# Optimization experiments

Measured on AMD Instinct MI355X. Metric: run time of the kernel, lower is better.

Reference implementation:

```python
import jax, jax.numpy as jnp
import numpy as np

# CTBG circuit dims: units=[512,512,512], action_sz=6
UNIT1, UNIT2, UNIT3, ACTION = 512, 512, 512, 6
D_GPE_IN = UNIT1 * 3          # 1536  (striatum D1/D2/D3 blocks)
D_GPE_OUT = UNIT2 * 3         # 1536
D_GPI_IN = (UNIT1 + UNIT2) * 3  # 3072 (striatum + GPe/STN blocks)
D_GPI_OUT = UNIT2 * 3         # 1536
B = 16384


def setup_inputs() -> dict:
    key = jax.random.key(0)
    ks = jax.random.split(key, 12)
    x = jax.random.normal(ks[0], (B, D_GPE_IN), jnp.float32)
    # per-unit diagonal connectivity masks (unit_diags): [units, input_dim]
    gpe_mask = jax.random.bernoulli(ks[1], 0.5, (D_GPE_OUT, D_GPE_IN)).astype(jnp.float32)
    gpi_mask = jax.random.bernoulli(ks[2], 0.5, (D_GPI_OUT, D_GPI_IN)).astype(jnp.float32)
    # non-negative weights, uniform [0, 0.01) as in the TF initializer
    gpe_w = jax.random.uniform(ks[3], (D_GPE_IN, D_GPE_OUT), jnp.float32, 0.0, 0.01)
    gpe_b = jnp.zeros((D_GPE_OUT,), jnp.float32)
    gpi_w = jax.random.uniform(ks[4], (D_GPI_IN, D_GPI_OUT), jnp.float32, 0.0, 0.01)
    gpi_b = jnp.zeros((D_GPI_OUT,), jnp.float32)
    # Motor_cortex dense stack
    w1 = jax.random.normal(ks[5], (D_GPI_OUT, UNIT3), jnp.float32) / np.sqrt(D_GPI_OUT)
    b1 = jnp.zeros((UNIT3,), jnp.float32)
    w2 = jax.random.normal(ks[6], (UNIT3, UNIT3), jnp.float32) / np.sqrt(UNIT3)
    b2 = jnp.zeros((UNIT3,), jnp.float32)
    w3 = jax.random.normal(ks[7], (UNIT3, ACTION), jnp.float32) / np.sqrt(UNIT3)
    b3 = jnp.zeros((ACTION,), jnp.float32)
    return {"x": x, "gpe_mask": gpe_mask, "gpe_w": gpe_w, "gpe_b": gpe_b,
            "gpi_mask": gpi_mask, "gpi_w": gpi_w, "gpi_b": gpi_b,
            "w1": w1, "b1": b1, "w2": w2, "b2": b2, "w3": w3, "b3": b3}


def _masked_layer(x, mask, w, b):
    # TF original: p = transpose(matmul(diag(mask_u), x^T)) -> [B,U,I];
    #              f = diag_part(matmul(p, w)) + b
    # algebraically: f[b,u] = sum_i mask[u,i] * x[b,i] * w[i,u] + b[u]
    # which is a plain matmul against the element-wise masked weight.
    return x @ (w * mask.T) + b


def reference(x, gpe_mask, gpe_w, gpe_b, gpi_mask, gpi_w, gpi_b,
              w1, b1, w2, b2, w3, b3):
    gpe_out = _masked_layer(x, gpe_mask, gpe_w, gpe_b)          # [B, 1536]
    gpi_in = jnp.concatenate([x, gpe_out], axis=-1)              # [B, 3072]
    gpi_out = _masked_layer(gpi_in, gpi_mask, gpi_w, gpi_b)      # [B, 1536]
    h = jax.nn.relu(gpi_out @ w1 + b1)
    h = jax.nn.relu(h @ w2 + b2)
    return jax.nn.relu(h @ w3 + b3)                              # [B, 6]
```

## Files before the change

### kernel.cpp

```cpp
#include <hip/hip_runtime.h>
#include <stdint.h>


typedef __attribute__((ext_vector_type(8))) short short8;
typedef __attribute__((ext_vector_type(4))) float floatx4;

typedef const __attribute__((address_space(1))) void* gas1_cvp;
typedef __attribute__((address_space(3))) void* gas3_vp;

__device__ __forceinline__ void load_lds16(const void* g, void* s) {
    __builtin_amdgcn_global_load_lds((gas1_cvp)g, (gas3_vp)s, 16, 0, 0);
}

__device__ __forceinline__ unsigned short f2bf(float f) {
    unsigned int u = __float_as_uint(f);
    u = u + 0x7fffu + ((u >> 16) & 1u);
    return (unsigned short)(u >> 16);
}
__device__ __forceinline__ float bf2f(unsigned short h) {
    return __uint_as_float(((unsigned int)h) << 16);
}
__device__ __forceinline__ short8 cvt8(float4 a, float4 b) {
    short8 r;
    r[0] = (short)f2bf(a.x); r[1] = (short)f2bf(a.y);
    r[2] = (short)f2bf(a.z); r[3] = (short)f2bf(a.w);
    r[4] = (short)f2bf(b.x); r[5] = (short)f2bf(b.y);
    r[6] = (short)f2bf(b.z); r[7] = (short)f2bf(b.w);
    return r;
}

__device__ __forceinline__ void dev_prep_t(
        float (*tile)[65],
        const float* __restrict__ w, const float* __restrict__ mask,
        unsigned short* __restrict__ out,
        int ldw, int ldm, int ldo, int bx, int by) {
    int n0 = bx * 64;
    int k0 = by * 64;
    int t = threadIdx.x;
    int c4 = (t & 15) * 4;
    int r  = t >> 4;

    #pragma unroll
    for (int p = 0; p < 4; ++p) {
        int kk = r + p * 16;
        float4 v = *(const float4*)(w + (size_t)(k0 + kk) * ldw + n0 + c4);
        tile[c4 + 0][kk] = v.x;
        tile[c4 + 1][kk] = v.y;
        tile[c4 + 2][kk] = v.z;
        tile[c4 + 3][kk] = v.w;
    }
    __syncthreads();
    #pragma unroll
    for (int p = 0; p < 4; ++p) {
        int nn = r + p * 16;
        float mx = 1.f, my = 1.f, mz = 1.f, mw = 1.f;
        if (mask) {
            float4 m = *(const float4*)(mask + (size_t)(n0 + nn) * ldm + k0 + c4);
            mx = m.x; my = m.y; mz = m.z; mw = m.w;
        }
        ushort4 o;
        o.x = f2bf(tile[nn][c4 + 0] * mx);
        o.y = f2bf(tile[nn][c4 + 1] * my);
        o.z = f2bf(tile[nn][c4 + 2] * mz);
        o.w = f2bf(tile[nn][c4 + 3] * mw);
        *(ushort4*)(out + (size_t)(n0 + nn) * ldo + k0 + c4) = o;
    }
}

__device__ __forceinline__ void dev_prep_nt(
        float (*tile)[65],
        const float* __restrict__ w, const float* __restrict__ mask,
        unsigned short* __restrict__ out,
        int ldw, int ldm, int ldo, int bx, int by) {
    int j0 = bx * 64;
    int i0 = by * 64;
    int t = threadIdx.x;
    int c4 = (t & 15) * 4;
    int r  = t >> 4;

    #pragma unroll
    for (int p = 0; p < 4; ++p) {
        int jj = r + p * 16;
        float4 m = *(const float4*)(mask + (size_t)(j0 + jj) * ldm + i0 + c4);
        tile[c4 + 0][jj] = m.x;
        tile[c4 + 1][jj] = m.y;
        tile[c4 + 2][jj] = m.z;
        tile[c4 + 3][jj] = m.w;
    }
    __syncthreads();
    #pragma unroll
    for (int p = 0; p < 4; ++p) {
        int ii = r + p * 16;
        float4 v = *(const float4*)(w + (size_t)(i0 + ii) * ldw + j0 + c4);
        ushort4 o;
        o.x = f2bf(v.x * tile[ii][c4 + 0]);
        o.y = f2bf(v.y * tile[ii][c4 + 1]);
        o.z = f2bf(v.z * tile[ii][c4 + 2]);
        o.w = f2bf(v.w * tile[ii][c4 + 3]);
        *(ushort4*)(out + (size_t)(i0 + ii) * ldo + j0 + c4) = o;
    }
}

__global__ __launch_bounds__(256) void prep_all_kernel(
        const float* __restrict__ gpe_w, const float* __restrict__ gpe_mask,
        const float* __restrict__ gpi_w, const float* __restrict__ gpi_mask,
        const float* __restrict__ w1, const float* __restrict__ w2,
        unsigned short* __restrict__ wi_topnt, unsigned short* __restrict__ wi_bot,
        unsigned short* __restrict__ we_nt, unsigned short* __restrict__ w1t,
        unsigned short* __restrict__ w2t) {
    __shared__ float tile[64][65];
    int b = blockIdx.x;
    if (b < 576) {
        dev_prep_nt(tile, gpi_w, gpi_mask, wi_topnt, 1536, 3072, 1536,
                    b % 24, b / 24);
    } else if (b < 1152) {
        int lb = b - 576;
        dev_prep_t(tile, gpi_w + (size_t)1536 * 1536, gpi_mask + 1536, wi_bot,
                   1536, 3072, 1536, lb % 24, lb / 24);
    } else if (b < 1728) {
        int lb = b - 1152;
        dev_prep_nt(tile, gpe_w, gpe_mask, we_nt, 1536, 1536, 1536,
                    lb % 24, lb / 24);
    } else if (b < 1920) {
        int lb = b - 1728;
        dev_prep_t(tile, w1, nullptr, w1t, 512, 0, 1536, lb % 8, lb / 8);
    } else {
        int lb = b - 1920;
        dev_prep_t(tile, w2, nullptr, w2t, 512, 0, 512, lb % 8, lb / 8);
    }
}

__device__ __forceinline__ void dev_bvec(
        const float* __restrict__ avec, const float* __restrict__ base,
        const unsigned short* __restrict__ wbt, float* __restrict__ outv,
        int K, int ld, int blk) {
    int u = blk * 4 + (threadIdx.x >> 6);
    int lane = threadIdx.x & 63;
    const unsigned short* rowp = wbt + (size_t)u * ld;
    float s = 0.f;
    for (int j = lane; j < K; j += 64) s += avec[j] * bf2f(rowp[j]);
    #pragma unroll
    for (int off = 32; off; off >>= 1) s += __shfl_down(s, off, 64);
    if (lane == 0) outv[u] = base[u] + s;
}

template <int BMODE>
__device__ __forceinline__ void dev_gemm64(
        unsigned short* As, unsigned short* Bs,
        const unsigned short* __restrict__ A,
        const unsigned short* __restrict__ Bt,
        const unsigned short* __restrict__ Add,
        unsigned short* __restrict__ C,
        int K, int lda, int ldc, int bx, int by) {
    const int m0 = by * 64;
    const int n0 = bx * 64;
    const int t    = threadIdx.x;
    const int lane = t & 63;
    const int w    = t >> 6;
    const int wm   = w >> 1;
    const int wn   = w & 1;
    const int lm   = lane & 15;
    const int lq   = lane >> 4;

    const int srow = lane >> 2;
    const int scol = (lane & 3) * 8;
    const unsigned short* ag = A  + (size_t)(m0 + w * 16 + srow) * lda + scol;
    const unsigned short* bg = Bt + (size_t)(n0 + w * 16 + srow) * K + scol;
    unsigned short* sA = As + w * 512;
    unsigned short* sB = Bs + w * 512;

    const unsigned short* arp[2];
    const unsigned short* brp[2];
    #pragma unroll
    for (int i = 0; i < 2; ++i) {
        arp[i] = As + (wm * 32 + i * 16 + lm) * 32 + lq * 8;
        brp[i] = Bs + (wn * 32 + i * 16 + lm) * 32 + lq * 8;
    }

    floatx4 acc[2][2] = {};

    for (int k0 = 0; k0 < K; k0 += 32) {
        __syncthreads();
        load_lds16(ag + k0, sA);
        load_lds16(bg + k0, sB);
        __syncthreads();

        short8 af[2], bf8[2];
        #pragma unroll
        for (int i = 0; i < 2; ++i) {
            af[i]  = *(const short8*)arp[i];
            bf8[i] = *(const short8*)brp[i];
        }
        #pragma unroll
        for (int mi = 0; mi < 2; ++mi)
            #pragma unroll
            for (int ni = 0; ni < 2; ++ni)
                acc[mi][ni] = __builtin_amdgcn_mfma_f32_16x16x32_bf16(
                    af[mi], bf8[ni], acc[mi][ni], 0, 0, 0);
    }

    #pragma unroll
    for (int mi = 0; mi < 2; ++mi) {
        int rbase = m0 + wm * 32 + mi * 16 + lq * 4;
        #pragma unroll
        for (int ni = 0; ni < 2; ++ni) {
            int cc = n0 + wn * 32 + ni * 16 + lm;
            #pragma unroll
            for (int r = 0; r < 4; ++r) {
                float v = acc[mi][ni][r];
                if (BMODE == 1) v += bf2f(Add[(size_t)(rbase + r) * ldc + cc]);
                C[(size_t)(rbase + r) * ldc + cc] = f2bf(v);
            }
        }
    }
}

__global__ __launch_bounds__(256) void combo1_kernel(
        const unsigned short* __restrict__ we_nt,
        const unsigned short* __restrict__ wi_bot,
        const unsigned short* __restrict__ wi_topnt,
        unsigned short* __restrict__ wc_nt,
        const float* __restrict__ gpe_b, const float* __restrict__ gpi_b,
        float* __restrict__ bc) {
    __shared__ unsigned short As[64 * 32];
    __shared__ unsigned short Bs[64 * 32];
    int b = blockIdx.x;
    if (b < 576) {
        dev_gemm64<1>(As, Bs, we_nt, wi_bot, wi_topnt, wc_nt,
                      1536, 1536, 1536, b % 24, b / 24);
    } else {
        dev_bvec(gpe_b, gpi_b, wi_bot, bc, 1536, 1536, b - 576);
    }
}

__global__ __launch_bounds__(256) void combo2_kernel(
        const unsigned short* __restrict__ w1t,
        const unsigned short* __restrict__ wc_nt,
        unsigned short* __restrict__ w1ct,
        const float* __restrict__ bc, const float* __restrict__ b1,
        float* __restrict__ b1c) {
    __shared__ unsigned short As[64 * 32];
    __shared__ unsigned short Bs[64 * 32];
    int b = blockIdx.x;
    if (b < 192) {
        dev_gemm64<2>(As, Bs, w1t, wc_nt, nullptr, w1ct,
                      1536, 1536, 1536, b % 24, b / 24);
    } else {
        dev_bvec(bc, b1, w1t, b1c, 1536, 1536, b - 192);
    }
}

__global__ __launch_bounds__(256) void gemm_a32_kernel(
        const float* __restrict__ A,
        const unsigned short* __restrict__ Bt,
        const float* __restrict__ bias,
        unsigned short* __restrict__ C,
        int K, int lda, int ldc) {
    __shared__ unsigned short As[128 * 32];
    __shared__ unsigned short Bs[128 * 32];

    const int m0 = blockIdx.y * 128;
    const int n0 = blockIdx.x * 128;
    const int t    = threadIdx.x;
    const int lane = t & 63;
    const int w    = t >> 6;
    const int wm   = w >> 1;
    const int wn   = w & 1;
    const int lm   = lane & 15;
    const int lq   = lane >> 4;

    const int srow = lane >> 2;
    const int scol = (lane & 3) * 8;
    const float* axg0 = A + (size_t)(m0 + w * 16 + srow) * lda + scol;
    const float* axg1 = A + (size_t)(m0 + (4 + w) * 16 + srow) * lda + scol;
    const unsigned short* bg0 = Bt + (size_t)(n0 + w * 16 + srow) * K + scol;
    const unsigned short* bg1 = Bt + (size_t)(n0 + (4 + w) * 16 + srow) * K + scol;
    unsigned short* sA0w = As + (w * 16 + srow) * 32 + scol;
    unsigned short* sA1w = As + ((4 + w) * 16 + srow) * 32 + scol;
    unsigned short* sB0 = Bs + w * 512;
    unsigned short* sB1 = Bs + (4 + w) * 512;

    const unsigned short* arp[4];
    const unsigned short* brp[4];
    #pragma unroll
    for (int i = 0; i < 4; ++i) {
        arp[i] = As + (wm * 64 + i * 16 + lm) * 32 + lq * 8;
        brp[i] = Bs + (wn * 64 + i * 16 + lm) * 32 + lq * 8;
    }

    floatx4 acc[4][4] = {};

    for (int k0 = 0; k0 < K; k0 += 32) {
        float4 a00 = *(const float4*)(axg0 + k0);
        float4 a01 = *(const float4*)(axg0 + k0 + 4);
        float4 a10 = *(const float4*)(axg1 + k0);
        float4 a11 = *(const float4*)(axg1 + k0 + 4);
        __syncthreads();
        load_lds16(bg0 + k0, sB0);
        load_lds16(bg1 + k0, sB1);
        *(short8*)sA0w = cvt8(a00, a01);
        *(short8*)sA1w = cvt8(a10, a11);
        __syncthreads();

        short8 af[4], bf8[4];
        #pragma unroll
        for (int i = 0; i < 4; ++i) {
            af[i]  = *(const short8*)arp[i];
            bf8[i] = *(const short8*)brp[i];
        }
        #pragma unroll
        for (int mi = 0; mi < 4; ++mi)
            #pragma unroll
            for (int ni = 0; ni < 4; ++ni)
                acc[mi][ni] = __builtin_amdgcn_mfma_f32_16x16x32_bf16(
                    af[mi], bf8[ni], acc[mi][ni], 0, 0, 0);
    }

    float bv[4];
    #pragma unroll
    for (int ni = 0; ni < 4; ++ni) bv[ni] = bias[n0 + wn * 64 + ni * 16 + lm];

    #pragma unroll
    for (int mi = 0; mi < 4; ++mi) {
        int rbase = m0 + wm * 64 + mi * 16 + lq * 4;
        #pragma unroll
        for (int ni = 0; ni < 4; ++ni) {
            int cc = n0 + wn * 64 + ni * 16 + lm;
            #pragma unroll
            for (int r = 0; r < 4; ++r) {
                float v = fmaxf(acc[mi][ni][r] + bv[ni], 0.f);
                C[(size_t)(rbase + r) * ldc + cc] = f2bf(v);
            }
        }
    }
}

__global__ __launch_bounds__(256) void gemm_bt_kernel(
        const unsigned short* __restrict__ A,
        const unsigned short* __restrict__ Bt,
        const float* __restrict__ bias,
        unsigned short* __restrict__ C,
        int K, int lda, int ldc) {
    __shared__ unsigned short As[128 * 32];
    __shared__ unsigned short Bs[128 * 32];

    const int m0 = blockIdx.y * 128;
    const int n0 = blockIdx.x * 128;
    const int t    = threadIdx.x;
    const int lane = t & 63;
    const int w    = t >> 6;
    const int wm   = w >> 1;
    const int wn   = w & 1;
    const int lm   = lane & 15;
    const int lq   = lane >> 4;

    const int srow = lane >> 2;
    const int scol = (lane & 3) * 8;
    const unsigned short* ag0 = A  + (size_t)(m0 + w * 16 + srow) * lda + scol;
    const unsigned short* ag1 = A  + (size_t)(m0 + (4 + w) * 16 + srow) * lda + scol;
    const unsigned short* bg0 = Bt + (size_t)(n0 + w * 16 + srow) * K + scol;
    const unsigned short* bg1 = Bt + (size_t)(n0 + (4 + w) * 16 + srow) * K + scol;
    unsigned short* sA0 = As + w * 512;
    unsigned short* sA1 = As + (4 + w) * 512;
    unsigned short* sB0 = Bs + w * 512;
    unsigned short* sB1 = Bs + (4 + w) * 512;

    const unsigned short* arp[4];
    const unsigned short* brp[4];
    #pragma unroll
    for (int i = 0; i < 4; ++i) {
        arp[i] = As + (wm * 64 + i * 16 + lm) * 32 + lq * 8;
        brp[i] = Bs + (wn * 64 + i * 16 + lm) * 32 + lq * 8;
    }

    floatx4 acc[4][4] = {};

    for (int k0 = 0; k0 < K; k0 += 32) {
        __syncthreads();
        load_lds16(ag0 + k0, sA0);
        load_lds16(ag1 + k0, sA1);
        load_lds16(bg0 + k0, sB0);
        load_lds16(bg1 + k0, sB1);
        __syncthreads();

        short8 af[4], bf8[4];
        #pragma unroll
        for (int i = 0; i < 4; ++i) {
            af[i]  = *(const short8*)arp[i];
            bf8[i] = *(const short8*)brp[i];
        }
        #pragma unroll
        for (int mi = 0; mi < 4; ++mi)
            #pragma unroll
            for (int ni = 0; ni < 4; ++ni)
                acc[mi][ni] = __builtin_amdgcn_mfma_f32_16x16x32_bf16(
                    af[mi], bf8[ni], acc[mi][ni], 0, 0, 0);
    }

    float bv[4];
    #pragma unroll
    for (int ni = 0; ni < 4; ++ni) bv[ni] = bias[n0 + wn * 64 + ni * 16 + lm];

    #pragma unroll
    for (int mi = 0; mi < 4; ++mi) {
        int rbase = m0 + wm * 64 + mi * 16 + lq * 4;
        #pragma unroll
        for (int ni = 0; ni < 4; ++ni) {
            int cc = n0 + wn * 64 + ni * 16 + lm;
            #pragma unroll
            for (int r = 0; r < 4; ++r) {
                float v = fmaxf(acc[mi][ni][r] + bv[ni], 0.f);
                C[(size_t)(rbase + r) * ldc + cc] = f2bf(v);
            }
        }
    }
}

__global__ void head_kernel(const unsigned short* __restrict__ h,
                            const float* __restrict__ w3,
                            const float* __restrict__ b3,
                            float* __restrict__ out) {
    int row = blockIdx.x * 4 + (threadIdx.x >> 6);
    int lane = threadIdx.x & 63;
    const unsigned short* hp = h + (size_t)row * 512 + lane * 8;
    ushort4 ha = *(const ushort4*)(hp);
    ushort4 hb = *(const ushort4*)(hp + 4);
    float hv[8] = {bf2f(ha.x), bf2f(ha.y), bf2f(ha.z), bf2f(ha.w),
                   bf2f(hb.x), bf2f(hb.y), bf2f(hb.z), bf2f(hb.w)};
    const float* wp = w3 + lane * 48;
    float s[6] = {0.f, 0.f, 0.f, 0.f, 0.f, 0.f};
    #pragma unroll
    for (int j = 0; j < 8; ++j)
        #pragma unroll
        for (int a = 0; a < 6; ++a)
            s[a] += hv[j] * wp[j * 6 + a];
    #pragma unroll
    for (int a = 0; a < 6; ++a)
        #pragma unroll
        for (int off = 32; off; off >>= 1)
            s[a] += __shfl_down(s[a], off, 64);
    if (lane == 0) {
        #pragma unroll
        for (int a = 0; a < 6; ++a)
            out[(size_t)row * 6 + a] = fmaxf(s[a] + b3[a], 0.f);
    }
}

extern "C" void kernel_launch(void* const* d_in, const int* in_sizes, int n_in,
                              void* d_out, int out_size, void* d_ws, size_t ws_size,
                              hipStream_t stream) {
    const float* x        = (const float*)d_in[0];
    const float* gpe_mask = (const float*)d_in[1];
    const float* gpe_w    = (const float*)d_in[2];
    const float* gpe_b    = (const float*)d_in[3];
    const float* gpi_mask = (const float*)d_in[4];
    const float* gpi_w    = (const float*)d_in[5];
    const float* gpi_b    = (const float*)d_in[6];
    const float* w1       = (const float*)d_in[7];
    const float* b1       = (const float*)d_in[8];
    const float* w2       = (const float*)d_in[9];
    const float* b2       = (const float*)d_in[10];
    const float* w3       = (const float*)d_in[11];
    const float* b3       = (const float*)d_in[12];
    float* out = (float*)d_out;

    char* ws = (char*)d_ws;
    unsigned short* h1        = (unsigned short*)(ws);
    unsigned short* h2        = (unsigned short*)(ws + 16777216);
    unsigned short* wi_topnt  = (unsigned short*)(ws + 33554432);
    unsigned short* wi_bot    = (unsigned short*)(ws + 38273024);
    unsigned short* we_nt     = (unsigned short*)(ws + 42991616);
    unsigned short* wc_nt     = (unsigned short*)(ws + 47710208);
    unsigned short* w1t       = (unsigned short*)(ws + 52428800);
    unsigned short* w2t       = (unsigned short*)(ws + 54001664);
    unsigned short* w1ct      = (unsigned short*)(ws + 54525952);
    float*          bc        = (float*)(ws + 56098816);
    float*          b1c       = (float*)(ws + 56104960);

    prep_all_kernel<<<dim3(1984), dim3(256), 0, stream>>>(
        gpe_w, gpe_mask, gpi_w, gpi_mask, w1, w2,
        wi_topnt, wi_bot, we_nt, w1t, w2t);

    combo1_kernel<<<dim3(960), dim3(256), 0, stream>>>(
        we_nt, wi_bot, wi_topnt, wc_nt, gpe_b, gpi_b, bc);

    combo2_kernel<<<dim3(320), dim3(256), 0, stream>>>(
        w1t, wc_nt, w1ct, bc, b1, b1c);

    gemm_a32_kernel<<<dim3(4, 128), dim3(256), 0, stream>>>(
        x, w1ct, b1c, h1, 1536, 1536, 512);
    gemm_bt_kernel<<<dim3(4, 128), dim3(256), 0, stream>>>(
        h1, w2t, b2, h2, 512, 512, 512);
    head_kernel<<<dim3(16384 / 4), dim3(256), 0, stream>>>(h2, w3, b3, out);
}
```

Before: 334.4 us.

## Retile fp32-input GEMM to full-width 32-row blocks so x is read once

Replaces the 128x128-tiled first GEMM, which read and converted each x row four times (once per N tile), with blocks covering 32 rows and all 512 output columns. Each x element is now read from fp32 global memory and converted to bf16 only once, and the next A chunk is prefetched into registers while the current one is processed. The trade-off is that every block streams the full 512x1536 weight matrix through LDS (32 KB of B per k-step), so weight traffic per row rises and only 512 blocks are launched, which lowers parallelism.

```diff
diff --git a/kernel.cpp b/kernel.cpp
--- a/kernel.cpp
+++ b/kernel.cpp
@@ -19,14 +19,6 @@
 }
 __device__ __forceinline__ float bf2f(unsigned short h) {
     return __uint_as_float(((unsigned int)h) << 16);
-}
-__device__ __forceinline__ short8 cvt8(float4 a, float4 b) {
-    short8 r;
-    r[0] = (short)f2bf(a.x); r[1] = (short)f2bf(a.y);
-    r[2] = (short)f2bf(a.z); r[3] = (short)f2bf(a.w);
-    r[4] = (short)f2bf(b.x); r[5] = (short)f2bf(b.y);
-    r[6] = (short)f2bf(b.z); r[7] = (short)f2bf(b.w);
-    return r;
 }
 
 __device__ __forceinline__ void dev_prep_t(
@@ -250,86 +242,79 @@
     }
 }
 
-__global__ __launch_bounds__(256) void gemm_a32_kernel(
+__global__ __launch_bounds__(256) void gemm_x32_kernel(
         const float* __restrict__ A,
         const unsigned short* __restrict__ Bt,
         const float* __restrict__ bias,
-        unsigned short* __restrict__ C,
-        int K, int lda, int ldc) {
-    __shared__ unsigned short As[128 * 32];
-    __shared__ unsigned short Bs[128 * 32];
-
-    const int m0 = blockIdx.y * 128;
-    const int n0 = blockIdx.x * 128;
+        unsigned short* __restrict__ C) {
+    __shared__ unsigned short As[32 * 32];
+    __shared__ unsigned short Bs[512 * 32];
+
+    const int m0   = blockIdx.x * 32;
     const int t    = threadIdx.x;
     const int lane = t & 63;
     const int w    = t >> 6;
-    const int wm   = w >> 1;
-    const int wn   = w & 1;
     const int lm   = lane & 15;
     const int lq   = lane >> 4;
 
+    const int arow = t >> 3;
+    const int acol = (t & 7) * 4;
+    const float* ag = A + (size_t)(m0 + arow) * 1536 + acol;
+    unsigned short* sAw = As + arow * 32 + acol;
+
     const int srow = lane >> 2;
     const int scol = (lane & 3) * 8;
-    const float* axg0 = A + (size_t)(m0 + w * 16 + srow) * lda + scol;
-    const float* axg1 = A + (size_t)(m0 + (4 + w) * 16 + srow) * lda + scol;
-    const unsigned short* bg0 = Bt + (size_t)(n0 + w * 16 + srow) * K + scol;
-    const unsigned short* bg1 = Bt + (size_t)(n0 + (4 + w) * 16 + srow) * K + scol;
-    unsigned short* sA0w = As + (w * 16 + srow) * 32 + scol;
-    unsigned short* sA1w = As + ((4 + w) * 16 + srow) * 32 + scol;
-    unsigned short* sB0 = Bs + w * 512;
-    unsigned short* sB1 = Bs + (4 + w) * 512;
-
-    const unsigned short* arp[4];
-    const unsigned short* brp[4];
-    #pragma unroll
-    for (int i = 0; i < 4; ++i) {
-        arp[i] = As + (wm * 64 + i * 16 + lm) * 32 + lq * 8;
-        brp[i] = Bs + (wn * 64 + i * 16 + lm) * 32 + lq * 8;
-    }
-
-    floatx4 acc[4][4] = {};
-
-    for (int k0 = 0; k0 < K; k0 += 32) {
-        float4 a00 = *(const float4*)(axg0 + k0);
-        float4 a01 = *(const float4*)(axg0 + k0 + 4);
-        float4 a10 = *(const float4*)(axg1 + k0);
-        float4 a11 = *(const float4*)(axg1 + k0 + 4);
-        __syncthreads();
-        load_lds16(bg0 + k0, sB0);
-        load_lds16(bg1 + k0, sB1);
-        *(short8*)sA0w = cvt8(a00, a01);
-        *(short8*)sA1w = cvt8(a10, a11);
-        __syncthreads();
-
-        short8 af[4], bf8[4];
-        #pragma unroll
-        for (int i = 0; i < 4; ++i) {
-            af[i]  = *(const short8*)arp[i];
-            bf8[i] = *(const short8*)brp[i];
-        }
-        #pragma unroll
-        for (int mi = 0; mi < 4; ++mi)
-            #pragma unroll
-            for (int ni = 0; ni < 4; ++ni)
+    const unsigned short* bg[8];
+    #pragma unroll
+    for (int c = 0; c < 8; ++c)
+        bg[c] = Bt + (size_t)(w * 128 + c * 16 + srow) * 1536 + scol;
+
+    floatx4 acc[2][8] = {};
+
+    float4 apre = *(const float4*)(ag);
+
+    for (int k0 = 0; k0 < 1536; k0 += 32) {
+        __syncthreads();
+        #pragma unroll
+        for (int c = 0; c < 8; ++c)
+            load_lds16(bg[c] + k0, Bs + (w * 128 + c * 16) * 32);
+        ushort4 o;
+        o.x = f2bf(apre.x); o.y = f2bf(apre.y);
+        o.z = f2bf(apre.z); o.w = f2bf(apre.w);
+        *(ushort4*)sAw = o;
+        int kn = (k0 + 32 < 1536) ? k0 + 32 : 0;
+        apre = *(const float4*)(ag + kn);
+        __syncthreads();
+
+        short8 af[2], bf8[8];
+        #pragma unroll
+        for (int i = 0; i < 2; ++i)
+            af[i] = *(const short8*)(As + (i * 16 + lm) * 32 + lq * 8);
+        #pragma unroll
+        for (int i = 0; i < 8; ++i)
+            bf8[i] = *(const short8*)(Bs + (w * 128 + i * 16 + lm) * 32 + lq * 8);
+        #pragma unroll
+        for (int mi = 0; mi < 2; ++mi)
+            #pragma unroll
+            for (int ni = 0; ni < 8; ++ni)
                 acc[mi][ni] = __builtin_amdgcn_mfma_f32_16x16x32_bf16(
                     af[mi], bf8[ni], acc[mi][ni], 0, 0, 0);
     }
 
-    float bv[4];
-    #pragma unroll
-    for (int ni = 0; ni < 4; ++ni) bv[ni] = bias[n0 + wn * 64 + ni * 16 + lm];
-
-    #pragma unroll
-    for (int mi = 0; mi < 4; ++mi) {
-        int rbase = m0 + wm * 64 + mi * 16 + lq * 4;
-        #pragma unroll
-        for (int ni = 0; ni < 4; ++ni) {
-            int cc = n0 + wn * 64 + ni * 16 + lm;
+    float bv[8];
+    #pragma unroll
+    for (int ni = 0; ni < 8; ++ni) bv[ni] = bias[w * 128 + ni * 16 + lm];
+
+    #pragma unroll
+    for (int mi = 0; mi < 2; ++mi) {
+        int rbase = m0 + mi * 16 + lq * 4;
+        #pragma unroll
+        for (int ni = 0; ni < 8; ++ni) {
+            int cc = w * 128 + ni * 16 + lm;
             #pragma unroll
             for (int r = 0; r < 4; ++r) {
                 float v = fmaxf(acc[mi][ni][r] + bv[ni], 0.f);
-                C[(size_t)(rbase + r) * ldc + cc] = f2bf(v);
+                C[(size_t)(rbase + r) * 512 + cc] = f2bf(v);
             }
         }
     }
@@ -487,8 +472,7 @@
     combo2_kernel<<<dim3(320), dim3(256), 0, stream>>>(
         w1t, wc_nt, w1ct, bc, b1, b1c);
 
-    gemm_a32_kernel<<<dim3(4, 128), dim3(256), 0, stream>>>(
-        x, w1ct, b1c, h1, 1536, 1536, 512);
+    gemm_x32_kernel<<<dim3(512), dim3(256), 0, stream>>>(x, w1ct, b1c, h1);
     gemm_bt_kernel<<<dim3(4, 128), dim3(256), 0, stream>>>(
         h1, w2t, b2, h2, 512, 512, 512);
     head_kernel<<<dim3(16384 / 4), dim3(256), 0, stream>>>(h2, w3, b3, out);
```

After: 346.5 us. 3.6% more time.
